# Kernel tuning notes

Measured on AMD Instinct MI355X. Metric: run time of the kernel, lower is better.

## Reference

```python
import jax, jax.numpy as jnp
import numpy as np

B, S, D, H, DFF = 2, 2048, 1024, 16, 4096
DK = D // H
EPS = 1e-6


def layer_norm(x, alpha, bias):
    # torch: alpha * (x - mean) / (std_unbiased + eps) + bias
    mean = jnp.mean(x, axis=-1, keepdims=True)
    std = jnp.sqrt(jnp.var(x, axis=-1, keepdims=True, ddof=1))
    return alpha * (x - mean) / (std + EPS) + bias


def setup_inputs() -> dict:
    key = jax.random.key(0)
    ks = jax.random.split(key, 10)
    w = lambda k, shape: (jax.random.normal(k, shape, jnp.float32) * 0.02)
    return {
        "x": jax.random.normal(ks[0], (B, S, D), jnp.float32),
        "mask": jnp.ones((B, 1, 1, S), jnp.int32),
        "wq": w(ks[1], (D, D)),
        "wk": w(ks[2], (D, D)),
        "wv": w(ks[3], (D, D)),
        "wo": w(ks[4], (D, D)),
        "w1": w(ks[5], (DFF, D)),
        "b1": jnp.zeros((DFF,), jnp.float32),
        "w2": w(ks[6], (D, DFF)),
        "b2": jnp.zeros((D,), jnp.float32),
        "alpha1": jnp.ones((D,), jnp.float32),
        "bias1": jnp.zeros((D,), jnp.float32),
        "alpha2": jnp.ones((D,), jnp.float32),
        "bias2": jnp.zeros((D,), jnp.float32),
    }


def reference(x, mask, wq, wk, wv, wo, w1, b1, w2, b2, alpha1, bias1, alpha2, bias2):
    # --- residual 1: pre-norm + self-attention ---
    xn = layer_norm(x, alpha1, bias1)                      # [B,S,D]
    q = (xn @ wq.T).reshape(B, S, H, DK).transpose(0, 2, 1, 3)  # [B,H,S,DK]
    k = (xn @ wk.T).reshape(B, S, H, DK).transpose(0, 2, 1, 3)
    v = (xn @ wv.T).reshape(B, S, H, DK).transpose(0, 2, 1, 3)
    scores = jnp.einsum("bhqd,bhkd->bhqk", q, k) / jnp.sqrt(jnp.float32(DK))
    scores = jnp.where(mask == 0, jnp.float32(-1e9), scores)
    attn = jax.nn.softmax(scores, axis=-1)                 # [B,H,S,S]
    av = jnp.einsum("bhqk,bhkd->bhqd", attn, v)            # [B,H,S,DK]
    av = av.transpose(0, 2, 1, 3).reshape(B, S, D)
    x = x + av @ wo.T                                      # dropout p=0
    # --- residual 2: pre-norm + FFN ---
    xn2 = layer_norm(x, alpha2, bias2)
    h = jax.nn.relu(xn2 @ w1.T + b1)                       # [B,S,DFF]
    x = x + h @ w2.T + b2
    return x
```

## Files before the change

kernel.cpp:

```cpp
#include <hip/hip_runtime.h>

#define B_   2
#define S_   2048
#define D_   1024
#define H_   16
#define DK_  64
#define DFF_ 4096
#define NTOK (B_ * S_)

#define QSCALE 0.18033688011112042f

typedef __bf16 bf16x8 __attribute__((ext_vector_type(8)));
typedef __bf16 bf16x4 __attribute__((ext_vector_type(4)));
typedef __bf16 bf16x2 __attribute__((ext_vector_type(2)));
typedef float  f32x4  __attribute__((ext_vector_type(4)));
typedef int    i32x4  __attribute__((ext_vector_type(4)));

#if __has_builtin(__builtin_amdgcn_exp2f)
#define EXP2(x) __builtin_amdgcn_exp2f(x)
#else
#define EXP2(x) exp2f(x)
#endif

__device__ __forceinline__ void ld16(const __bf16* g, __bf16* l) {
  __builtin_amdgcn_global_load_lds(
      (const __attribute__((address_space(1))) void*)g,
      (__attribute__((address_space(3))) void*)l, 16, 0, 0);
}

#define RAW_BAR()     __asm__ __volatile__("s_barrier" ::: "memory")
#define SCHED_FENCE() __builtin_amdgcn_sched_barrier(0)

__device__ __forceinline__ int packbf(float lo, float hi) {
  bf16x2 r; r[0] = (__bf16)lo; r[1] = (__bf16)hi;
  return __builtin_bit_cast(int, r);
}

__device__ __forceinline__ void swap32(int a, int b, int& g0, int& g1, bool hi32) {
#if __has_builtin(__builtin_amdgcn_permlane32_swap)
  auto r = __builtin_amdgcn_permlane32_swap(a, b, false, false);
  g0 = r[0]; g1 = r[1];
  (void)hi32;
#else
  const int sa = __builtin_amdgcn_ds_swizzle(a, 0x801F);
  const int sb = __builtin_amdgcn_ds_swizzle(b, 0x801F);
  g0 = hi32 ? sb : a;
  g1 = hi32 ? b : sa;
#endif
}

__device__ __forceinline__ void swap16(int a, int b, int& h0, int& h1, bool hi16) {
#if __has_builtin(__builtin_amdgcn_permlane16_swap)
  auto r = __builtin_amdgcn_permlane16_swap(a, b, false, false);
  h0 = r[0]; h1 = r[1];
  (void)hi16;
#else
  const int sa = __builtin_amdgcn_ds_swizzle(a, 0x401F);
  const int sb = __builtin_amdgcn_ds_swizzle(b, 0x401F);
  h0 = hi16 ? sb : a;
  h1 = hi16 ? b : sa;
#endif
}

__device__ __forceinline__ void xcd_swz256(int& bx, int& by) {
  const int gx = gridDim.x;
  const int flat = blockIdx.y * gx + blockIdx.x;
  const int x = flat & 7, n = flat >> 3;
  if (gx == 16) { by = ((x >> 1) << 2) + (n >> 3); bx = ((x & 1) << 3) + (n & 7); }
  else          { by = (x << 1) + (n >> 2);        bx = n & 3; }
}

__device__ __forceinline__ void lda4(bf16x8 (&afr)[4], const __bf16* hb,
                                     int abase, int f0) {
#pragma unroll
  for (int i = 0; i < 4; ++i)
    afr[i] = *(const bf16x8*)(hb + abase + (f0 + i) * 512);
}

__device__ __forceinline__ void ldb4(bf16x8 (&bfr)[4], const __bf16* hb,
                                     int bbase) {
#pragma unroll
  for (int j = 0; j < 4; ++j)
    bfr[j] = *(const bf16x8*)(hb + bbase + j * 512);
}

__device__ __forceinline__ void mm16(f32x4 (&acc)[8][4], const bf16x8 (&afr)[4],
                                     const bf16x8 (&bfr)[4], int r0) {
#pragma unroll
  for (int i = 0; i < 4; ++i)
#pragma unroll
    for (int j = 0; j < 4; ++j)
      acc[r0 + i][j] =
          __builtin_amdgcn_mfma_f32_16x16x32_bf16(afr[i], bfr[j], acc[r0 + i][j], 0, 0, 0);
}

__device__ __forceinline__ void gemm_core_256(
    const __bf16* __restrict__ A, const __bf16* __restrict__ W,
    int ld, int kLen, int rowA0, int rowW0,
    f32x4 (&acc)[8][4], __bf16* Ls)
{
  const int t = threadIdx.x;
  const int lane = t & 63, wv = t >> 6;
  const int wm = wv >> 2, wn = wv & 3;
  const int l15 = lane & 15, q4 = lane >> 4;

  const int lane_rd = l15 * 32 + ((q4 * 8) ^ (((l15 >> 1) & 3) << 3));
  const int abase = wm * 4096 + lane_rd;
  const int bbase = wn * 2048 + lane_rd;

  const int sc0 = t ^ ((t >> 3) & 3);
  const __bf16* gA0 = A + (size_t)(rowA0 + (sc0 >> 2)) * ld + (sc0 & 3) * 8;
  const __bf16* gA1 = gA0 + (size_t)128 * ld;
  const __bf16* gW0 = W + (size_t)(rowW0 + (sc0 >> 2)) * ld + (sc0 & 3) * 8;
  const __bf16* gW1 = gW0 + (size_t)128 * ld;
  const int d0 = wv * 512, d1 = 4096 + wv * 512;

#pragma unroll
  for (int i = 0; i < 8; ++i)
#pragma unroll
    for (int j = 0; j < 4; ++j) acc[i][j] = (f32x4){0.f, 0.f, 0.f, 0.f};

#define HBASE(slot, mat, h) (Ls + ((((slot)*2) + (mat)) * 2 + (h)) * 8192)
#define STG_A(tt, h, slot) do { __bf16* _d = HBASE(slot, 0, h);              \
    const int _ko = (tt) * 64 + (h) * 32;                                    \
    ld16(gA0 + _ko, _d + d0); ld16(gA1 + _ko, _d + d1); } while (0)
#define STG_B(tt, h, slot) do { __bf16* _d = HBASE(slot, 1, h);              \
    const int _ko = (tt) * 64 + (h) * 32;                                    \
    ld16(gW0 + _ko, _d + d0); ld16(gW1 + _ko, _d + d1); } while (0)
#define MFMA_PH(r0) do { RAW_BAR(); SCHED_FENCE();                           \
    __builtin_amdgcn_s_setprio(1); mm16(acc, afr, bfr, r0);                  \
    __builtin_amdgcn_s_setprio(0); SCHED_FENCE(); RAW_BAR(); } while (0)

  const int NT = kLen >> 6;
  bf16x8 afr[4], bfr[4];

  STG_A(0, 0, 0); STG_A(0, 1, 0); STG_B(0, 0, 0); STG_B(0, 1, 0);
  STG_B(1, 0, 1); STG_A(1, 0, 1); STG_B(1, 1, 1);
  __asm__ __volatile__("s_waitcnt vmcnt(6)" ::: "memory");
  RAW_BAR(); SCHED_FENCE();

  for (int u = 0; u < NT; u += 2) {
    const bool g2 = (u + 2) < NT, g3 = (u + 3) < NT;
    lda4(afr, HBASE(0, 0, 0), abase, 0); ldb4(bfr, HBASE(0, 1, 0), bbase);
    STG_A(u + 1, 1, 1);
    MFMA_PH(0);
    lda4(afr, HBASE(0, 0, 0), abase, 4);
    if (g2) STG_B(u + 2, 0, 0);
    MFMA_PH(4);
    lda4(afr, HBASE(0, 0, 1), abase, 0); ldb4(bfr, HBASE(0, 1, 1), bbase);
    if (g2) STG_A(u + 2, 0, 0);
    MFMA_PH(0);
    lda4(afr, HBASE(0, 0, 1), abase, 4);
    if (g2) {
      STG_B(u + 2, 1, 0);
      __asm__ __volatile__("s_waitcnt vmcnt(6)" ::: "memory");
    } else {
      __asm__ __volatile__("s_waitcnt vmcnt(0)" ::: "memory");
    }
    MFMA_PH(4);
    lda4(afr, HBASE(1, 0, 0), abase, 0); ldb4(bfr, HBASE(1, 1, 0), bbase);
    if (g2) STG_A(u + 2, 1, 0);
    MFMA_PH(0);
    lda4(afr, HBASE(1, 0, 0), abase, 4);
    if (g3) STG_B(u + 3, 0, 1);
    MFMA_PH(4);
    lda4(afr, HBASE(1, 0, 1), abase, 0); ldb4(bfr, HBASE(1, 1, 1), bbase);
    if (g3) STG_A(u + 3, 0, 1);
    MFMA_PH(0);
    lda4(afr, HBASE(1, 0, 1), abase, 4);
    if (g3) STG_B(u + 3, 1, 1);
    __asm__ __volatile__("s_waitcnt vmcnt(6)" ::: "memory");
    MFMA_PH(4);
  }
#undef HBASE
#undef STG_A
#undef STG_B
#undef MFMA_PH
}

__global__ __launch_bounds__(512, 2) void gemm_qkv_256(
    const __bf16* __restrict__ xn,
    const __bf16* __restrict__ wqb, const __bf16* __restrict__ wkb,
    const __bf16* __restrict__ wvb,
    __bf16* __restrict__ qo, __bf16* __restrict__ ko, __bf16* __restrict__ vto)
{
  __shared__ __align__(16) __bf16 Ls[65536];
  int bx, by; xcd_swz256(bx, by);
  const __bf16* W = blockIdx.z == 0 ? wqb : (blockIdx.z == 1 ? wkb : wvb);
  f32x4 acc[8][4];
  gemm_core_256(xn, W, D_, D_, by * 256, bx * 256, acc, Ls);

  const int t = threadIdx.x, lane = t & 63, wv = t >> 6;
  const int wm = wv >> 2, wn = wv & 3;
  const int l15 = lane & 15, q4 = lane >> 4;
  const int row0 = by * 256 + wm * 128;
  const int col0 = bx * 256 + wn * 64;

  if (blockIdx.z < 2) {
    __bf16* o = blockIdx.z == 0 ? qo : ko;
    const float sc = blockIdx.z == 0 ? QSCALE : 1.0f;
#pragma unroll
    for (int fr = 0; fr < 8; ++fr)
#pragma unroll
      for (int fc = 0; fc < 4; ++fc) {
        const int col = col0 + fc * 16 + l15;
#pragma unroll
        for (int r = 0; r < 4; ++r) {
          const int row = row0 + fr * 16 + q4 * 4 + r;
          o[(size_t)row * D_ + col] = (__bf16)(acc[fr][fc][r] * sc);
        }
      }
  } else {
#pragma unroll
    for (int fr = 0; fr < 8; ++fr)
#pragma unroll
      for (int fc = 0; fc < 4; ++fc) {
        const int tok0 = row0 + fr * 16 + q4 * 4;
        const int c    = col0 + fc * 16 + l15;
        const int b0 = tok0 >> 11, s0 = tok0 & (S_ - 1);
        const int hh = c >> 6, dd = c & (DK_ - 1);
        bf16x4 pk;
#pragma unroll
        for (int r = 0; r < 4; ++r) pk[r] = (__bf16)acc[fr][fc][r];
        *(bf16x4*)&vto[(size_t)((b0 * H_ + hh) * DK_ + dd) * S_ + s0] = pk;
      }
  }
}

__global__ __launch_bounds__(512, 2) void gemm_ffn1_256(
    const __bf16* __restrict__ A, const __bf16* __restrict__ W,
    __bf16* __restrict__ outb, const float* __restrict__ bias)
{
  __shared__ __align__(16) __bf16 Ls[65536];
  int bx, by; xcd_swz256(bx, by);
  f32x4 acc[8][4];
  gemm_core_256(A, W, D_, D_, by * 256, bx * 256, acc, Ls);

  const int t = threadIdx.x, lane = t & 63, wv = t >> 6;
  const int wm = wv >> 2, wn = wv & 3;
  const int l15 = lane & 15, q4 = lane >> 4;
  const int row0 = by * 256 + wm * 128;
  const int col0 = bx * 256 + wn * 64;

#pragma unroll
  for (int fr = 0; fr < 8; ++fr)
#pragma unroll
    for (int fc = 0; fc < 4; ++fc) {
      const int col = col0 + fc * 16 + l15;
      const float bs = bias[col];
#pragma unroll
      for (int r = 0; r < 4; ++r) {
        const int row = row0 + fr * 16 + q4 * 4 + r;
        outb[(size_t)row * DFF_ + col] = (__bf16)fmaxf(acc[fr][fc][r] + bs, 0.0f);
      }
    }
}

__global__ __launch_bounds__(512, 2) void gemm_ffn2_sk4(
    const __bf16* __restrict__ A, const __bf16* __restrict__ W,
    __bf16* __restrict__ p0, __bf16* __restrict__ p1,
    __bf16* __restrict__ p2, __bf16* __restrict__ p3)
{
  __shared__ __align__(16) __bf16 Ls[65536];
  int bx, by; xcd_swz256(bx, by);
  const int z = blockIdx.z;
  f32x4 acc[8][4];
  gemm_core_256(A + (size_t)z * 1024, W + (size_t)z * 1024, DFF_, 1024,
                by * 256, bx * 256, acc, Ls);

  const int t = threadIdx.x, lane = t & 63, wv = t >> 6;
  const int wm = wv >> 2, wn = wv & 3;
  const int l15 = lane & 15, q4 = lane >> 4;
  const int row0 = by * 256 + wm * 128;
  const int col0 = bx * 256 + wn * 64;
  __bf16* out = z == 0 ? p0 : (z == 1 ? p1 : (z == 2 ? p2 : p3));

#pragma unroll
  for (int fr = 0; fr < 8; ++fr)
#pragma unroll
    for (int fc = 0; fc < 4; ++fc) {
      const int col = col0 + fc * 16 + l15;
#pragma unroll
      for (int r = 0; r < 4; ++r) {
        const int row = row0 + fr * 16 + q4 * 4 + r;
        out[(size_t)row * D_ + col] = (__bf16)acc[fr][fc][r];
      }
    }
}

__global__ __launch_bounds__(512, 2) void gemm_oproj_sk4(
    const __bf16* __restrict__ A, const __bf16* __restrict__ W,
    __bf16* __restrict__ pp)
{
  __shared__ __align__(16) __bf16 Ls[65536];
  int bx, by; xcd_swz256(bx, by);
  const int z = blockIdx.z;
  f32x4 acc[8][4];
  gemm_core_256(A + (size_t)z * 256, W + (size_t)z * 256, D_, 256,
                by * 256, bx * 256, acc, Ls);

  const int t = threadIdx.x, lane = t & 63, wv = t >> 6;
  const int wm = wv >> 2, wn = wv & 3;
  const int l15 = lane & 15, q4 = lane >> 4;
  const int row0 = by * 256 + wm * 128;
  const int col0 = bx * 256 + wn * 64;
  __bf16* out = pp + (size_t)z * NTOK * D_;

#pragma unroll
  for (int fr = 0; fr < 8; ++fr)
#pragma unroll
    for (int fc = 0; fc < 4; ++fc) {
      const int col = col0 + fc * 16 + l15;
#pragma unroll
      for (int r = 0; r < 4; ++r) {
        const int row = row0 + fr * 16 + q4 * 4 + r;
        out[(size_t)row * D_ + col] = (__bf16)acc[fr][fc][r];
      }
    }
}

__global__ __launch_bounds__(256) void oproj_ln_reduce(
    const float* __restrict__ x, const __bf16* __restrict__ opp,
    const float* __restrict__ alpha, const float* __restrict__ bias,
    const float* __restrict__ b2, float* __restrict__ dout,
    __bf16* __restrict__ xn2)
{
  const int row = blockIdx.x;
  const int t = threadIdx.x;
  const size_t base = (size_t)row * D_;
  const size_t st4 = (size_t)NTOK * D_ / 4;
  const size_t i4 = base / 4 + t;
  float4 v = ((const float4*)(x + base))[t];
  const bf16x4 a0 = ((const bf16x4*)opp)[i4];
  const bf16x4 a1 = ((const bf16x4*)opp)[i4 + st4];
  const bf16x4 a2 = ((const bf16x4*)opp)[i4 + 2 * st4];
  const bf16x4 a3 = ((const bf16x4*)opp)[i4 + 3 * st4];
  v.x += (float)a0[0] + (float)a1[0] + (float)a2[0] + (float)a3[0];
  v.y += (float)a0[1] + (float)a1[1] + (float)a2[1] + (float)a3[1];
  v.z += (float)a0[2] + (float)a1[2] + (float)a2[2] + (float)a3[2];
  v.w += (float)a0[3] + (float)a1[3] + (float)a2[3] + (float)a3[3];

  const float4 bb = ((const float4*)b2)[t];
  float4 o4;
  o4.x = v.x + bb.x; o4.y = v.y + bb.y; o4.z = v.z + bb.z; o4.w = v.w + bb.w;
  ((float4*)(dout + base))[t] = o4;

  float s  = v.x + v.y + v.z + v.w;
  float ss = v.x * v.x + v.y * v.y + v.z * v.z + v.w * v.w;
#pragma unroll
  for (int m = 1; m < 64; m <<= 1) {
    s  += __shfl_xor(s, m);
    ss += __shfl_xor(ss, m);
  }
  __shared__ float red[8];
  if ((t & 63) == 0) { red[t >> 6] = s; red[4 + (t >> 6)] = ss; }
  __syncthreads();
  s  = red[0] + red[1] + red[2] + red[3];
  ss = red[4] + red[5] + red[6] + red[7];
  const float mean = s * (1.0f / D_);
  float var = (ss - (float)D_ * mean * mean) * (1.0f / (D_ - 1));
  var = fmaxf(var, 0.0f);
  const float inv = 1.0f / (sqrtf(var) + 1e-6f);
  const float4 al = ((const float4*)alpha)[t];
  const float4 bi = ((const float4*)bias)[t];
  bf16x4 o;
  o.x = (__bf16)(al.x * (v.x - mean) * inv + bi.x);
  o.y = (__bf16)(al.y * (v.y - mean) * inv + bi.y);
  o.z = (__bf16)(al.z * (v.z - mean) * inv + bi.z);
  o.w = (__bf16)(al.w * (v.w - mean) * inv + bi.w);
  ((bf16x4*)(xn2 + base))[t] = o;
}

__global__ __launch_bounds__(256) void ffn2_reduce(
    const __bf16* __restrict__ p0, const __bf16* __restrict__ p1,
    const __bf16* __restrict__ p2, const __bf16* __restrict__ p3,
    float* __restrict__ out)
{
  const int idx4 = blockIdx.x * 256 + threadIdx.x;
  float4 v = ((const float4*)out)[idx4];
  const bf16x4 q0 = ((const bf16x4*)p0)[idx4];
  const bf16x4 q1 = ((const bf16x4*)p1)[idx4];
  const bf16x4 q2 = ((const bf16x4*)p2)[idx4];
  const bf16x4 q3 = ((const bf16x4*)p3)[idx4];
  v.x += (float)q0[0] + (float)q1[0] + (float)q2[0] + (float)q3[0];
  v.y += (float)q0[1] + (float)q1[1] + (float)q2[1] + (float)q3[1];
  v.z += (float)q0[2] + (float)q1[2] + (float)q2[2] + (float)q3[2];
  v.w += (float)q0[3] + (float)q1[3] + (float)q2[3] + (float)q3[3];
  ((float4*)out)[idx4] = v;
}

struct CastJobs {
  const float* src[6];
  __bf16* dst[6];
  int n4[6];
};

__global__ __launch_bounds__(256) void cast_ln_kernel(
    CastJobs cj, const float* __restrict__ x, const float* __restrict__ alpha,
    const float* __restrict__ bias, __bf16* __restrict__ xn1)
{
  const int j = blockIdx.y;
  if (j < 6) {
    const int i = blockIdx.x * 256 + threadIdx.x;
    if (i < cj.n4[j]) {
      float4 v = ((const float4*)cj.src[j])[i];
      bf16x4 o;
      o.x = (__bf16)v.x; o.y = (__bf16)v.y; o.z = (__bf16)v.z; o.w = (__bf16)v.w;
      ((bf16x4*)cj.dst[j])[i] = o;
    }
    return;
  }
  const int row = blockIdx.x;
  const int t = threadIdx.x;
  const float4 v = ((const float4*)(x + (size_t)row * D_))[t];
  float s  = v.x + v.y + v.z + v.w;
  float ss = v.x * v.x + v.y * v.y + v.z * v.z + v.w * v.w;
#pragma unroll
  for (int m = 1; m < 64; m <<= 1) {
    s  += __shfl_xor(s, m);
    ss += __shfl_xor(ss, m);
  }
  __shared__ float red[8];
  if ((t & 63) == 0) { red[t >> 6] = s; red[4 + (t >> 6)] = ss; }
  __syncthreads();
  s  = red[0] + red[1] + red[2] + red[3];
  ss = red[4] + red[5] + red[6] + red[7];
  const float mean = s * (1.0f / D_);
  float var = (ss - (float)D_ * mean * mean) * (1.0f / (D_ - 1));
  var = fmaxf(var, 0.0f);
  const float inv = 1.0f / (sqrtf(var) + 1e-6f);
  const float4 al = ((const float4*)alpha)[t];
  const float4 bi = ((const float4*)bias)[t];
  bf16x4 o;
  o.x = (__bf16)(al.x * (v.x - mean) * inv + bi.x);
  o.y = (__bf16)(al.y * (v.y - mean) * inv + bi.y);
  o.z = (__bf16)(al.z * (v.z - mean) * inv + bi.z);
  o.w = (__bf16)(al.w * (v.w - mean) * inv + bi.w);
  ((bf16x4*)(xn1 + (size_t)row * D_))[t] = o;
}

__global__ __launch_bounds__(256) void attn_kernel(
    const __bf16* __restrict__ qg, const __bf16* __restrict__ kg,
    const __bf16* __restrict__ vtg, const int* __restrict__ mask,
    __bf16* __restrict__ av)
{
  __shared__ __align__(16) __bf16 Ks[2][4096];
  __shared__ __align__(16) __bf16 Vt[2][4096];
  __shared__ __align__(16) __bf16 Qs[8192];
  __shared__ int Dd[32];

  const int t = threadIdx.x, lane = t & 63, wv = t >> 6;
  const int l15 = lane & 15, q4 = lane >> 4;
  const bool hi16 = (lane & 16) != 0, hi32 = (lane & 32) != 0;
  const int bh = blockIdx.x;
  const int b = bh >> 4, h = bh & (H_ - 1);
  const int q0 = blockIdx.y * 128;

  const int srow = lane & 7, sc8 = lane >> 3;
  const __bf16* qg0 = qg + (size_t)(b * S_ + q0 + 32 * wv + srow) * D_ + h * DK_ + sc8 * 8;
  __bf16* lQ = Qs + wv * 2048;
#pragma unroll
  for (int p = 0; p < 4; ++p)
    ld16(qg0 + (size_t)(8 * p) * D_, lQ + 512 * p);

  const __bf16* kg0 = kg + (size_t)(b * S_ + 16 * wv + srow) * D_ + h * DK_ + sc8 * 8;
  const __bf16* vt0 = vtg + (size_t)(bh * DK_ + 16 * wv + srow) * S_ + sc8 * 8;

  if (t < 32) Dd[t] = 0;

  ld16(kg0,                  Ks[0] + wv * 1024);
  ld16(kg0 + (size_t)8 * D_, Ks[0] + wv * 1024 + 512);
  ld16(vt0,                  Vt[0] + wv * 1024);
  ld16(vt0 + (size_t)8 * S_, Vt[0] + wv * 1024 + 512);

  __syncthreads();

  {
    const int4* m4 = (const int4*)(mask + (size_t)b * S_) + t * 2;
    const int4 a = m4[0], c = m4[1];
    const bool anyz = (a.x == 0) | (a.y == 0) | (a.z == 0) | (a.w == 0) |
                      (c.x == 0) | (c.y == 0) | (c.z == 0) | (c.w == 0);
    if (anyz) Dd[t >> 3] = 1;
  }
  __syncthreads();
  const bool blockDirty = (__ballot(Dd[lane & 31] != 0) != 0ull);

  const int fb = ((l15 >> 3) << 9) + (q4 << 6) + ((l15 & 7) << 3);
  const int mrow = b * S_;

  bf16x8 bq[2][2];
#pragma unroll
  for (int j = 0; j < 2; ++j)
#pragma unroll
    for (int s = 0; s < 2; ++s)
      bq[j][s] = *(const bf16x8*)(lQ + j * 1024 + s * 256 + fb);

  bf16x8 bones;
#pragma unroll
  for (int e = 0; e < 8; ++e) bones[e] = (__bf16)1.0f;
  const f32x4 z4 = {0.f, 0.f, 0.f, 0.f};

  f32x4 lacc[2];
  f32x4 oacc[2][4];
#pragma unroll
  for (int m = 0; m < 2; ++m) {
    lacc[m] = z4;
#pragma unroll
    for (int jd = 0; jd < 4; ++jd) oacc[m][jd] = z4;
  }

  for (int kv0 = 0; kv0 < S_; kv0 += 64) {
    const int buf = (kv0 >> 6) & 1;
    if (kv0 + 64 < S_) {
      const size_t nk = (size_t)(kv0 + 64);
      ld16(kg0 + nk * D_,              Ks[buf ^ 1] + wv * 1024);
      ld16(kg0 + (nk + 8) * D_,        Ks[buf ^ 1] + wv * 1024 + 512);
      ld16(vt0 + nk,                   Vt[buf ^ 1] + wv * 1024);
      ld16(vt0 + (size_t)8 * S_ + nk,  Vt[buf ^ 1] + wv * 1024 + 512);
    }

    f32x4 sacc[4][2];
    __builtin_amdgcn_s_setprio(1);
#pragma unroll
    for (int i = 0; i < 4; ++i) {
      const bf16x8 ak0 = *(const bf16x8*)(Ks[buf] + i * 1024 + fb);
      const bf16x8 ak1 = *(const bf16x8*)(Ks[buf] + i * 1024 + fb + 256);
      sacc[i][0] = __builtin_amdgcn_mfma_f32_16x16x32_bf16(ak0, bq[0][0], z4, 0, 0, 0);
      sacc[i][1] = __builtin_amdgcn_mfma_f32_16x16x32_bf16(ak0, bq[1][0], z4, 0, 0, 0);
      sacc[i][0] = __builtin_amdgcn_mfma_f32_16x16x32_bf16(ak1, bq[0][1], sacc[i][0], 0, 0, 0);
      sacc[i][1] = __builtin_amdgcn_mfma_f32_16x16x32_bf16(ak1, bq[1][1], sacc[i][1], 0, 0, 0);
    }
    __builtin_amdgcn_s_setprio(0);

    if (blockDirty && Dd[kv0 >> 6]) {
#pragma unroll
      for (int i = 0; i < 4; ++i)
#pragma unroll
        for (int r = 0; r < 4; ++r)
          if (mask[mrow + kv0 + 16 * i + 4 * q4 + r] == 0) {
            sacc[i][0][r] = -1e30f;
            sacc[i][1][r] = -1e30f;
          }
    }

#pragma unroll
    for (int i = 0; i < 4; ++i)
#pragma unroll
      for (int j = 0; j < 2; ++j)
#pragma unroll
        for (int r = 0; r < 4; ++r)
          sacc[i][j][r] = EXP2(sacc[i][j][r]);

    bf16x8 ap[2][2];
#pragma unroll
    for (int j = 0; j < 2; ++j)
#pragma unroll
      for (int s = 0; s < 2; ++s) {
        const int pa0 = packbf(sacc[2 * s][j][0],     sacc[2 * s][j][1]);
        const int pa1 = packbf(sacc[2 * s][j][2],     sacc[2 * s][j][3]);
        const int pb0 = packbf(sacc[2 * s + 1][j][0], sacc[2 * s + 1][j][1]);
        const int pb1 = packbf(sacc[2 * s + 1][j][2], sacc[2 * s + 1][j][3]);
        int g0, g1, g2, g3, h0, h1, h2, h3;
        swap32(pa0, pb0, g0, g1, hi32);
        swap32(pa1, pb1, g2, g3, hi32);
        swap16(g0, g1, h0, h1, hi16);
        swap16(g2, g3, h2, h3, hi16);
        i32x4 fw; fw[0] = h0; fw[1] = h2; fw[2] = h1; fw[3] = h3;
        ap[j][s] = __builtin_bit_cast(bf16x8, fw);
      }

    __builtin_amdgcn_s_setprio(1);
#pragma unroll
    for (int jd = 0; jd < 4; ++jd)
#pragma unroll
      for (int s = 0; s < 2; ++s) {
        bf16x8 bv = *(const bf16x8*)(Vt[buf] + jd * 1024 + fb + s * 256);
#pragma unroll
        for (int m = 0; m < 2; ++m)
          oacc[m][jd] = __builtin_amdgcn_mfma_f32_16x16x32_bf16(ap[m][s], bv, oacc[m][jd], 0, 0, 0);
      }
#pragma unroll
    for (int m = 0; m < 2; ++m)
#pragma unroll
      for (int s = 0; s < 2; ++s)
        lacc[m] = __builtin_amdgcn_mfma_f32_16x16x32_bf16(ap[m][s], bones, lacc[m], 0, 0, 0);
    __builtin_amdgcn_s_setprio(0);

    __syncthreads();
  }

#pragma unroll
  for (int m = 0; m < 2; ++m) {
    f32x4 lt;
#pragma unroll
    for (int r = 0; r < 4; ++r) lt[r] = 1.0f / lacc[m][r];
#pragma unroll
    for (int jd = 0; jd < 4; ++jd)
#pragma unroll
      for (int r = 0; r < 4; ++r) {
        int tok = b * S_ + q0 + wv * 32 + 16 * m + q4 * 4 + r;
        int c   = h * DK_ + jd * 16 + l15;
        av[(size_t)tok * D_ + c] = (__bf16)(oacc[m][jd][r] * lt[r]);
      }
  }
}

extern "C" void kernel_launch(void* const* d_in, const int* in_sizes, int n_in,
                              void* d_out, int out_size, void* d_ws, size_t ws_size,
                              hipStream_t stream) {
  const float* x      = (const float*)d_in[0];
  const int*   mask   = (const int*)d_in[1];
  const float* wq     = (const float*)d_in[2];
  const float* wk     = (const float*)d_in[3];
  const float* wv     = (const float*)d_in[4];
  const float* wo     = (const float*)d_in[5];
  const float* w1     = (const float*)d_in[6];
  const float* b1     = (const float*)d_in[7];
  const float* w2     = (const float*)d_in[8];
  const float* b2     = (const float*)d_in[9];
  const float* alpha1 = (const float*)d_in[10];
  const float* bias1  = (const float*)d_in[11];
  const float* alpha2 = (const float*)d_in[12];
  const float* bias2  = (const float*)d_in[13];

  char* ws = (char*)d_ws;
  __bf16* wqb = (__bf16*)(ws + ((size_t)0 << 20));
  __bf16* wkb = (__bf16*)(ws + ((size_t)2 << 20));
  __bf16* wvb = (__bf16*)(ws + ((size_t)4 << 20));
  __bf16* wob = (__bf16*)(ws + ((size_t)6 << 20));
  __bf16* w1b = (__bf16*)(ws + ((size_t)8 << 20));
  __bf16* w2b = (__bf16*)(ws + ((size_t)16 << 20));
  __bf16* xn1 = (__bf16*)(ws + ((size_t)24 << 20));
  __bf16* qb  = (__bf16*)(ws + ((size_t)32 << 20));
  __bf16* kb  = (__bf16*)(ws + ((size_t)40 << 20));
  __bf16* vtb = (__bf16*)(ws + ((size_t)48 << 20));
  __bf16* avb = (__bf16*)(ws + ((size_t)56 << 20));
  __bf16* opp = (__bf16*)(ws + ((size_t)24 << 20));
  __bf16* xn2 = (__bf16*)(ws + ((size_t)56 << 20));
  __bf16* hb  = (__bf16*)(ws + ((size_t)24 << 20));
  __bf16* fp0 = (__bf16*)(ws + ((size_t)0 << 20));
  __bf16* fp1 = (__bf16*)(ws + ((size_t)8 << 20));
  __bf16* fp2 = (__bf16*)(ws + ((size_t)56 << 20));
  __bf16* fp3 = (__bf16*)(ws + ((size_t)64 << 20));

  CastJobs cj;
  cj.src[0] = wq; cj.dst[0] = wqb; cj.n4[0] = D_ * D_ / 4;
  cj.src[1] = wk; cj.dst[1] = wkb; cj.n4[1] = D_ * D_ / 4;
  cj.src[2] = wv; cj.dst[2] = wvb; cj.n4[2] = D_ * D_ / 4;
  cj.src[3] = wo; cj.dst[3] = wob; cj.n4[3] = D_ * D_ / 4;
  cj.src[4] = w1; cj.dst[4] = w1b; cj.n4[4] = DFF_ * D_ / 4;
  cj.src[5] = w2; cj.dst[5] = w2b; cj.n4[5] = DFF_ * D_ / 4;

  cast_ln_kernel<<<dim3(DFF_ * D_ / 4 / 256, 7), 256, 0, stream>>>(
      cj, x, alpha1, bias1, xn1);

  gemm_qkv_256<<<dim3(D_ / 256, NTOK / 256, 3), 512, 0, stream>>>(
      xn1, wqb, wkb, wvb, qb, kb, vtb);

  attn_kernel<<<dim3(B_ * H_, S_ / 128), 256, 0, stream>>>(qb, kb, vtb, mask, avb);

  gemm_oproj_sk4<<<dim3(D_ / 256, NTOK / 256, 4), 512, 0, stream>>>(
      avb, wob, opp);

  oproj_ln_reduce<<<dim3(NTOK), 256, 0, stream>>>(
      x, opp, alpha2, bias2, b2, (float*)d_out, xn2);

  gemm_ffn1_256<<<dim3(DFF_ / 256, NTOK / 256), 512, 0, stream>>>(
      xn2, w1b, hb, b1);

  gemm_ffn2_sk4<<<dim3(D_ / 256, NTOK / 256, 4), 512, 0, stream>>>(
      hb, w2b, fp0, fp1, fp2, fp3);

  ffn2_reduce<<<dim3(NTOK * D_ / 4 / 256), 256, 0, stream>>>(
      fp0, fp1, fp2, fp3, (float*)d_out);
}
```

Before: 322.6 us.

## Software-pipeline attention with triple-buffered K/V and QK of next tile ahead

Restructures the attention kv loop so the QK^T MFMAs for tile i+1 are issued while softmax/exp and PV for tile i run, using two score register sets. K/V shared buffers grow to three so prefetch runs two tiles ahead, and the Q shared-memory staging is dropped in favor of direct global loads into registers. It also replaces the per-iteration __syncthreads with an explicit vmcnt wait plus raw barrier. This raises register pressure (two score sets) and LDS use per block, which could lower occupancy.

```diff
diff --git a/kernel.cpp b/kernel.cpp
--- a/kernel.cpp
+++ b/kernel.cpp
@@ -444,9 +444,8 @@
     const __bf16* __restrict__ vtg, const int* __restrict__ mask,
     __bf16* __restrict__ av)
 {
-  __shared__ __align__(16) __bf16 Ks[2][4096];
-  __shared__ __align__(16) __bf16 Vt[2][4096];
-  __shared__ __align__(16) __bf16 Qs[8192];
+  __shared__ __align__(16) __bf16 Ks[3][4096];
+  __shared__ __align__(16) __bf16 Vt[3][4096];
   __shared__ int Dd[32];
 
   const int t = threadIdx.x, lane = t & 63, wv = t >> 6;
@@ -455,23 +454,21 @@
   const int bh = blockIdx.x;
   const int b = bh >> 4, h = bh & (H_ - 1);
   const int q0 = blockIdx.y * 128;
-
   const int srow = lane & 7, sc8 = lane >> 3;
-  const __bf16* qg0 = qg + (size_t)(b * S_ + q0 + 32 * wv + srow) * D_ + h * DK_ + sc8 * 8;
-  __bf16* lQ = Qs + wv * 2048;
-#pragma unroll
-  for (int p = 0; p < 4; ++p)
-    ld16(qg0 + (size_t)(8 * p) * D_, lQ + 512 * p);
 
   const __bf16* kg0 = kg + (size_t)(b * S_ + 16 * wv + srow) * D_ + h * DK_ + sc8 * 8;
   const __bf16* vt0 = vtg + (size_t)(bh * DK_ + 16 * wv + srow) * S_ + sc8 * 8;
 
   if (t < 32) Dd[t] = 0;
 
-  ld16(kg0,                  Ks[0] + wv * 1024);
-  ld16(kg0 + (size_t)8 * D_, Ks[0] + wv * 1024 + 512);
-  ld16(vt0,                  Vt[0] + wv * 1024);
-  ld16(vt0 + (size_t)8 * S_, Vt[0] + wv * 1024 + 512);
+  ld16(kg0,                       Ks[0] + wv * 1024);
+  ld16(kg0 + (size_t)8 * D_,      Ks[0] + wv * 1024 + 512);
+  ld16(vt0,                       Vt[0] + wv * 1024);
+  ld16(vt0 + (size_t)8 * S_,      Vt[0] + wv * 1024 + 512);
+  ld16(kg0 + (size_t)64 * D_,     Ks[1] + wv * 1024);
+  ld16(kg0 + (size_t)72 * D_,     Ks[1] + wv * 1024 + 512);
+  ld16(vt0 + 64,                  Vt[1] + wv * 1024);
+  ld16(vt0 + (size_t)8 * S_ + 64, Vt[1] + wv * 1024 + 512);
 
   __syncthreads();
 
@@ -493,7 +490,8 @@
   for (int j = 0; j < 2; ++j)
 #pragma unroll
     for (int s = 0; s < 2; ++s)
-      bq[j][s] = *(const bf16x8*)(lQ + j * 1024 + s * 256 + fb);
+      bq[j][s] = *(const bf16x8*)(qg +
+          (size_t)(b * S_ + q0 + 32 * wv + j * 16 + l15) * D_ + h * DK_ + s * 32 + q4 * 8);
 
   bf16x8 bones;
 #pragma unroll
@@ -509,85 +507,103 @@
     for (int jd = 0; jd < 4; ++jd) oacc[m][jd] = z4;
   }
 
-  for (int kv0 = 0; kv0 < S_; kv0 += 64) {
-    const int buf = (kv0 >> 6) & 1;
-    if (kv0 + 64 < S_) {
-      const size_t nk = (size_t)(kv0 + 64);
-      ld16(kg0 + nk * D_,              Ks[buf ^ 1] + wv * 1024);
-      ld16(kg0 + (nk + 8) * D_,        Ks[buf ^ 1] + wv * 1024 + 512);
-      ld16(vt0 + nk,                   Vt[buf ^ 1] + wv * 1024);
-      ld16(vt0 + (size_t)8 * S_ + nk,  Vt[buf ^ 1] + wv * 1024 + 512);
-    }
-
-    f32x4 sacc[4][2];
-    __builtin_amdgcn_s_setprio(1);
-#pragma unroll
-    for (int i = 0; i < 4; ++i) {
-      const bf16x8 ak0 = *(const bf16x8*)(Ks[buf] + i * 1024 + fb);
-      const bf16x8 ak1 = *(const bf16x8*)(Ks[buf] + i * 1024 + fb + 256);
-      sacc[i][0] = __builtin_amdgcn_mfma_f32_16x16x32_bf16(ak0, bq[0][0], z4, 0, 0, 0);
-      sacc[i][1] = __builtin_amdgcn_mfma_f32_16x16x32_bf16(ak0, bq[1][0], z4, 0, 0, 0);
-      sacc[i][0] = __builtin_amdgcn_mfma_f32_16x16x32_bf16(ak1, bq[0][1], sacc[i][0], 0, 0, 0);
-      sacc[i][1] = __builtin_amdgcn_mfma_f32_16x16x32_bf16(ak1, bq[1][1], sacc[i][1], 0, 0, 0);
-    }
-    __builtin_amdgcn_s_setprio(0);
-
-    if (blockDirty && Dd[kv0 >> 6]) {
-#pragma unroll
-      for (int i = 0; i < 4; ++i)
-#pragma unroll
-        for (int r = 0; r < 4; ++r)
-          if (mask[mrow + kv0 + 16 * i + 4 * q4 + r] == 0) {
-            sacc[i][0][r] = -1e30f;
-            sacc[i][1][r] = -1e30f;
-          }
-    }
-
-#pragma unroll
-    for (int i = 0; i < 4; ++i)
-#pragma unroll
-      for (int j = 0; j < 2; ++j)
-#pragma unroll
-        for (int r = 0; r < 4; ++r)
-          sacc[i][j][r] = EXP2(sacc[i][j][r]);
-
-    bf16x8 ap[2][2];
-#pragma unroll
-    for (int j = 0; j < 2; ++j)
-#pragma unroll
-      for (int s = 0; s < 2; ++s) {
-        const int pa0 = packbf(sacc[2 * s][j][0],     sacc[2 * s][j][1]);
-        const int pa1 = packbf(sacc[2 * s][j][2],     sacc[2 * s][j][3]);
-        const int pb0 = packbf(sacc[2 * s + 1][j][0], sacc[2 * s + 1][j][1]);
-        const int pb1 = packbf(sacc[2 * s + 1][j][2], sacc[2 * s + 1][j][3]);
-        int g0, g1, g2, g3, h0, h1, h2, h3;
-        swap32(pa0, pb0, g0, g1, hi32);
-        swap32(pa1, pb1, g2, g3, hi32);
-        swap16(g0, g1, h0, h1, hi16);
-        swap16(g2, g3, h2, h3, hi16);
-        i32x4 fw; fw[0] = h0; fw[1] = h2; fw[2] = h1; fw[3] = h3;
-        ap[j][s] = __builtin_bit_cast(bf16x8, fw);
-      }
-
-    __builtin_amdgcn_s_setprio(1);
-#pragma unroll
-    for (int jd = 0; jd < 4; ++jd)
-#pragma unroll
-      for (int s = 0; s < 2; ++s) {
-        bf16x8 bv = *(const bf16x8*)(Vt[buf] + jd * 1024 + fb + s * 256);
-#pragma unroll
-        for (int m = 0; m < 2; ++m)
-          oacc[m][jd] = __builtin_amdgcn_mfma_f32_16x16x32_bf16(ap[m][s], bv, oacc[m][jd], 0, 0, 0);
-      }
-#pragma unroll
-    for (int m = 0; m < 2; ++m)
-#pragma unroll
-      for (int s = 0; s < 2; ++s)
-        lacc[m] = __builtin_amdgcn_mfma_f32_16x16x32_bf16(ap[m][s], bones, lacc[m], 0, 0, 0);
-    __builtin_amdgcn_s_setprio(0);
-
-    __syncthreads();
-  }
+  const __bf16 *kC = Ks[0], *kN = Ks[1], *vC = Vt[0], *vN = Vt[1];
+  __bf16 *kP = Ks[2], *vP = Vt[2];
+
+  f32x4 sA[4][2], sB[4][2];
+
+#pragma unroll
+  for (int i = 0; i < 4; ++i) {
+    const bf16x8 ak0 = *(const bf16x8*)(kC + i * 1024 + fb);
+    const bf16x8 ak1 = *(const bf16x8*)(kC + i * 1024 + fb + 256);
+    sA[i][0] = __builtin_amdgcn_mfma_f32_16x16x32_bf16(ak0, bq[0][0], z4, 0, 0, 0);
+    sA[i][1] = __builtin_amdgcn_mfma_f32_16x16x32_bf16(ak0, bq[1][0], z4, 0, 0, 0);
+    sA[i][0] = __builtin_amdgcn_mfma_f32_16x16x32_bf16(ak1, bq[0][1], sA[i][0], 0, 0, 0);
+    sA[i][1] = __builtin_amdgcn_mfma_f32_16x16x32_bf16(ak1, bq[1][1], sA[i][1], 0, 0, 0);
+  }
+
+#define ATTN_BODY(IT, SIN, SOUT)                                              \
+  do {                                                                        \
+    const int kv0_ = (IT) * 64;                                               \
+    if (kv0_ + 128 < S_) {                 \
+      const size_t nk_ = (size_t)(kv0_ + 128);                                \
+      ld16(kg0 + nk_ * D_,             kP + wv * 1024);                       \
+      ld16(kg0 + (nk_ + 8) * D_,       kP + wv * 1024 + 512);                 \
+      ld16(vt0 + nk_,                  vP + wv * 1024);                       \
+      ld16(vt0 + (size_t)8 * S_ + nk_, vP + wv * 1024 + 512);                 \
+    }                                                                         \
+    if (kv0_ + 64 < S_) {                       \
+      _Pragma("unroll")                                                       \
+      for (int i_ = 0; i_ < 4; ++i_) {                                        \
+        const bf16x8 ak0_ = *(const bf16x8*)(kN + i_ * 1024 + fb);            \
+        const bf16x8 ak1_ = *(const bf16x8*)(kN + i_ * 1024 + fb + 256);      \
+        SOUT[i_][0] = __builtin_amdgcn_mfma_f32_16x16x32_bf16(ak0_, bq[0][0], z4, 0, 0, 0); \
+        SOUT[i_][1] = __builtin_amdgcn_mfma_f32_16x16x32_bf16(ak0_, bq[1][0], z4, 0, 0, 0); \
+        SOUT[i_][0] = __builtin_amdgcn_mfma_f32_16x16x32_bf16(ak1_, bq[0][1], SOUT[i_][0], 0, 0, 0); \
+        SOUT[i_][1] = __builtin_amdgcn_mfma_f32_16x16x32_bf16(ak1_, bq[1][1], SOUT[i_][1], 0, 0, 0); \
+      }                                                                       \
+    }                                                                         \
+    if (blockDirty && Dd[(IT)]) {                                             \
+      _Pragma("unroll")                                                       \
+      for (int i_ = 0; i_ < 4; ++i_)                                          \
+        _Pragma("unroll")                                                     \
+        for (int r_ = 0; r_ < 4; ++r_)                                        \
+          if (mask[mrow + kv0_ + 16 * i_ + 4 * q4 + r_] == 0) {               \
+            SIN[i_][0][r_] = -1e30f;                                          \
+            SIN[i_][1][r_] = -1e30f;                                          \
+          }                                                                   \
+    }                                                                         \
+    _Pragma("unroll")                                                         \
+    for (int i_ = 0; i_ < 4; ++i_)                                            \
+      _Pragma("unroll")                                                       \
+      for (int j_ = 0; j_ < 2; ++j_)                                          \
+        _Pragma("unroll")                                                     \
+        for (int r_ = 0; r_ < 4; ++r_)                                        \
+          SIN[i_][j_][r_] = EXP2(SIN[i_][j_][r_]);                            \
+    bf16x8 ap_[2][2];                                                         \
+    _Pragma("unroll")                                                         \
+    for (int j_ = 0; j_ < 2; ++j_)                                            \
+      _Pragma("unroll")                                                       \
+      for (int s_ = 0; s_ < 2; ++s_) {                                        \
+        const int pa0_ = packbf(SIN[2 * s_][j_][0],     SIN[2 * s_][j_][1]);  \
+        const int pa1_ = packbf(SIN[2 * s_][j_][2],     SIN[2 * s_][j_][3]);  \
+        const int pb0_ = packbf(SIN[2 * s_ + 1][j_][0], SIN[2 * s_ + 1][j_][1]); \
+        const int pb1_ = packbf(SIN[2 * s_ + 1][j_][2], SIN[2 * s_ + 1][j_][3]); \
+        int g0_, g1_, g2_, g3_, h0_, h1_, h2_, h3_;                           \
+        swap32(pa0_, pb0_, g0_, g1_, hi32);                                   \
+        swap32(pa1_, pb1_, g2_, g3_, hi32);                                   \
+        swap16(g0_, g1_, h0_, h1_, hi16);                                     \
+        swap16(g2_, g3_, h2_, h3_, hi16);                                     \
+        i32x4 fw_; fw_[0] = h0_; fw_[1] = h2_; fw_[2] = h1_; fw_[3] = h3_;    \
+        ap_[j_][s_] = __builtin_bit_cast(bf16x8, fw_);                        \
+      }                                                                       \
+    __builtin_amdgcn_s_setprio(1);                                            \
+    _Pragma("unroll")                                                         \
+    for (int jd_ = 0; jd_ < 4; ++jd_)                                         \
+      _Pragma("unroll")                                                       \
+      for (int s_ = 0; s_ < 2; ++s_) {                                        \
+        bf16x8 bv_ = *(const bf16x8*)(vC + jd_ * 1024 + fb + s_ * 256);       \
+        _Pragma("unroll")                                                     \
+        for (int m_ = 0; m_ < 2; ++m_)                                        \
+          oacc[m_][jd_] = __builtin_amdgcn_mfma_f32_16x16x32_bf16(ap_[m_][s_], bv_, oacc[m_][jd_], 0, 0, 0); \
+      }                                                                       \
+    _Pragma("unroll")                                                         \
+    for (int m_ = 0; m_ < 2; ++m_)                                            \
+      _Pragma("unroll")                                                       \
+      for (int s_ = 0; s_ < 2; ++s_)                                          \
+        lacc[m_] = __builtin_amdgcn_mfma_f32_16x16x32_bf16(ap_[m_][s_], bones, lacc[m_], 0, 0, 0); \
+    __builtin_amdgcn_s_setprio(0);                                            \
+    __asm__ __volatile__("s_waitcnt vmcnt(0)" ::: "memory");                  \
+    RAW_BAR();                                                                \
+    const __bf16* tk_ = kC; kC = kN; kN = kP; kP = (__bf16*)tk_;              \
+    const __bf16* tv_ = vC; vC = vN; vN = vP; vP = (__bf16*)tv_;              \
+  } while (0)
+
+  for (int it = 0; it < 32; it += 2) {
+    ATTN_BODY(it,     sA, sB);
+    ATTN_BODY(it + 1, sB, sA);
+  }
+#undef ATTN_BODY
 
 #pragma unroll
   for (int m = 0; m < 2; ++m) {
```

Result: slower. 333.6 us (+3.4%).

## Halve attention query tile per block to raise occupancy and block count

Applied to the files above, without the earlier changes.

The attention kernel now processes 64 queries per block (16 per wave) instead of 128, doubling the grid to 1024 blocks and removing the Q shared-memory staging in favor of direct global loads into registers. Launch bounds request 4 blocks per CU, and register and LDS usage per block drop. The trade-off is that each K/V tile loaded into LDS is reused by half as many queries, doubling total K/V traffic and the per-query share of synchronization.

```diff
diff --git a/kernel.cpp b/kernel.cpp
--- a/kernel.cpp
+++ b/kernel.cpp
@@ -439,14 +439,13 @@
   ((bf16x4*)(xn1 + (size_t)row * D_))[t] = o;
 }
 
-__global__ __launch_bounds__(256) void attn_kernel(
+__global__ __launch_bounds__(256, 4) void attn_kernel(
     const __bf16* __restrict__ qg, const __bf16* __restrict__ kg,
     const __bf16* __restrict__ vtg, const int* __restrict__ mask,
     __bf16* __restrict__ av)
 {
   __shared__ __align__(16) __bf16 Ks[2][4096];
   __shared__ __align__(16) __bf16 Vt[2][4096];
-  __shared__ __align__(16) __bf16 Qs[8192];
   __shared__ int Dd[32];
 
   const int t = threadIdx.x, lane = t & 63, wv = t >> 6;
@@ -454,14 +453,8 @@
   const bool hi16 = (lane & 16) != 0, hi32 = (lane & 32) != 0;
   const int bh = blockIdx.x;
   const int b = bh >> 4, h = bh & (H_ - 1);
-  const int q0 = blockIdx.y * 128;
-
+  const int q0 = blockIdx.y * 64;
   const int srow = lane & 7, sc8 = lane >> 3;
-  const __bf16* qg0 = qg + (size_t)(b * S_ + q0 + 32 * wv + srow) * D_ + h * DK_ + sc8 * 8;
-  __bf16* lQ = Qs + wv * 2048;
-#pragma unroll
-  for (int p = 0; p < 4; ++p)
-    ld16(qg0 + (size_t)(8 * p) * D_, lQ + 512 * p);
 
   const __bf16* kg0 = kg + (size_t)(b * S_ + 16 * wv + srow) * D_ + h * DK_ + sc8 * 8;
   const __bf16* vt0 = vtg + (size_t)(bh * DK_ + 16 * wv + srow) * S_ + sc8 * 8;
@@ -488,26 +481,21 @@
   const int fb = ((l15 >> 3) << 9) + (q4 << 6) + ((l15 & 7) << 3);
   const int mrow = b * S_;
 
-  bf16x8 bq[2][2];
-#pragma unroll
-  for (int j = 0; j < 2; ++j)
-#pragma unroll
-    for (int s = 0; s < 2; ++s)
-      bq[j][s] = *(const bf16x8*)(lQ + j * 1024 + s * 256 + fb);
+  bf16x8 bq[2];
+#pragma unroll
+  for (int s = 0; s < 2; ++s)
+    bq[s] = *(const bf16x8*)(qg +
+        (size_t)(b * S_ + q0 + 16 * wv + l15) * D_ + h * DK_ + s * 32 + q4 * 8);
 
   bf16x8 bones;
 #pragma unroll
   for (int e = 0; e < 8; ++e) bones[e] = (__bf16)1.0f;
   const f32x4 z4 = {0.f, 0.f, 0.f, 0.f};
 
-  f32x4 lacc[2];
-  f32x4 oacc[2][4];
-#pragma unroll
-  for (int m = 0; m < 2; ++m) {
-    lacc[m] = z4;
-#pragma unroll
-    for (int jd = 0; jd < 4; ++jd) oacc[m][jd] = z4;
-  }
+  f32x4 lacc = z4;
+  f32x4 oacc[4];
+#pragma unroll
+  for (int jd = 0; jd < 4; ++jd) oacc[jd] = z4;
 
   for (int kv0 = 0; kv0 < S_; kv0 += 64) {
     const int buf = (kv0 >> 6) & 1;
@@ -519,16 +507,14 @@
       ld16(vt0 + (size_t)8 * S_ + nk,  Vt[buf ^ 1] + wv * 1024 + 512);
     }
 
-    f32x4 sacc[4][2];
+    f32x4 sacc[4];
     __builtin_amdgcn_s_setprio(1);
 #pragma unroll
     for (int i = 0; i < 4; ++i) {
       const bf16x8 ak0 = *(const bf16x8*)(Ks[buf] + i * 1024 + fb);
       const bf16x8 ak1 = *(const bf16x8*)(Ks[buf] + i * 1024 + fb + 256);
-      sacc[i][0] = __builtin_amdgcn_mfma_f32_16x16x32_bf16(ak0, bq[0][0], z4, 0, 0, 0);
-      sacc[i][1] = __builtin_amdgcn_mfma_f32_16x16x32_bf16(ak0, bq[1][0], z4, 0, 0, 0);
-      sacc[i][0] = __builtin_amdgcn_mfma_f32_16x16x32_bf16(ak1, bq[0][1], sacc[i][0], 0, 0, 0);
-      sacc[i][1] = __builtin_amdgcn_mfma_f32_16x16x32_bf16(ak1, bq[1][1], sacc[i][1], 0, 0, 0);
+      sacc[i] = __builtin_amdgcn_mfma_f32_16x16x32_bf16(ak0, bq[0], z4, 0, 0, 0);
+      sacc[i] = __builtin_amdgcn_mfma_f32_16x16x32_bf16(ak1, bq[1], sacc[i], 0, 0, 0);
     }
     __builtin_amdgcn_s_setprio(0);
 
@@ -537,37 +523,31 @@
       for (int i = 0; i < 4; ++i)
 #pragma unroll
         for (int r = 0; r < 4; ++r)
-          if (mask[mrow + kv0 + 16 * i + 4 * q4 + r] == 0) {
-            sacc[i][0][r] = -1e30f;
-            sacc[i][1][r] = -1e30f;
-          }
+          if (mask[mrow + kv0 + 16 * i + 4 * q4 + r] == 0)
+            sacc[i][r] = -1e30f;
     }
 
 #pragma unroll
     for (int i = 0; i < 4; ++i)
 #pragma unroll
-      for (int j = 0; j < 2; ++j)
-#pragma unroll
-        for (int r = 0; r < 4; ++r)
-          sacc[i][j][r] = EXP2(sacc[i][j][r]);
-
-    bf16x8 ap[2][2];
-#pragma unroll
-    for (int j = 0; j < 2; ++j)
-#pragma unroll
-      for (int s = 0; s < 2; ++s) {
-        const int pa0 = packbf(sacc[2 * s][j][0],     sacc[2 * s][j][1]);
-        const int pa1 = packbf(sacc[2 * s][j][2],     sacc[2 * s][j][3]);
-        const int pb0 = packbf(sacc[2 * s + 1][j][0], sacc[2 * s + 1][j][1]);
-        const int pb1 = packbf(sacc[2 * s + 1][j][2], sacc[2 * s + 1][j][3]);
-        int g0, g1, g2, g3, h0, h1, h2, h3;
-        swap32(pa0, pb0, g0, g1, hi32);
-        swap32(pa1, pb1, g2, g3, hi32);
-        swap16(g0, g1, h0, h1, hi16);
-        swap16(g2, g3, h2, h3, hi16);
-        i32x4 fw; fw[0] = h0; fw[1] = h2; fw[2] = h1; fw[3] = h3;
-        ap[j][s] = __builtin_bit_cast(bf16x8, fw);
-      }
+      for (int r = 0; r < 4; ++r)
+        sacc[i][r] = EXP2(sacc[i][r]);
+
+    bf16x8 ap[2];
+#pragma unroll
+    for (int s = 0; s < 2; ++s) {
+      const int pa0 = packbf(sacc[2 * s][0],     sacc[2 * s][1]);
+      const int pa1 = packbf(sacc[2 * s][2],     sacc[2 * s][3]);
+      const int pb0 = packbf(sacc[2 * s + 1][0], sacc[2 * s + 1][1]);
+      const int pb1 = packbf(sacc[2 * s + 1][2], sacc[2 * s + 1][3]);
+      int g0, g1, g2, g3, h0, h1, h2, h3;
+      swap32(pa0, pb0, g0, g1, hi32);
+      swap32(pa1, pb1, g2, g3, hi32);
+      swap16(g0, g1, h0, h1, hi16);
+      swap16(g2, g3, h2, h3, hi16);
+      i32x4 fw; fw[0] = h0; fw[1] = h2; fw[2] = h1; fw[3] = h3;
+      ap[s] = __builtin_bit_cast(bf16x8, fw);
+    }
 
     __builtin_amdgcn_s_setprio(1);
 #pragma unroll
@@ -575,34 +555,27 @@
 #pragma unroll
       for (int s = 0; s < 2; ++s) {
         bf16x8 bv = *(const bf16x8*)(Vt[buf] + jd * 1024 + fb + s * 256);
-#pragma unroll
-        for (int m = 0; m < 2; ++m)
-          oacc[m][jd] = __builtin_amdgcn_mfma_f32_16x16x32_bf16(ap[m][s], bv, oacc[m][jd], 0, 0, 0);
+        oacc[jd] = __builtin_amdgcn_mfma_f32_16x16x32_bf16(ap[s], bv, oacc[jd], 0, 0, 0);
       }
 #pragma unroll
-    for (int m = 0; m < 2; ++m)
-#pragma unroll
-      for (int s = 0; s < 2; ++s)
-        lacc[m] = __builtin_amdgcn_mfma_f32_16x16x32_bf16(ap[m][s], bones, lacc[m], 0, 0, 0);
+    for (int s = 0; s < 2; ++s)
+      lacc = __builtin_amdgcn_mfma_f32_16x16x32_bf16(ap[s], bones, lacc, 0, 0, 0);
     __builtin_amdgcn_s_setprio(0);
 
     __syncthreads();
   }
 
-#pragma unroll
-  for (int m = 0; m < 2; ++m) {
-    f32x4 lt;
-#pragma unroll
-    for (int r = 0; r < 4; ++r) lt[r] = 1.0f / lacc[m][r];
-#pragma unroll
-    for (int jd = 0; jd < 4; ++jd)
-#pragma unroll
-      for (int r = 0; r < 4; ++r) {
-        int tok = b * S_ + q0 + wv * 32 + 16 * m + q4 * 4 + r;
-        int c   = h * DK_ + jd * 16 + l15;
-        av[(size_t)tok * D_ + c] = (__bf16)(oacc[m][jd][r] * lt[r]);
-      }
-  }
+  f32x4 lt;
+#pragma unroll
+  for (int r = 0; r < 4; ++r) lt[r] = 1.0f / lacc[r];
+#pragma unroll
+  for (int jd = 0; jd < 4; ++jd)
+#pragma unroll
+    for (int r = 0; r < 4; ++r) {
+      int tok = b * S_ + q0 + 16 * wv + q4 * 4 + r;
+      int c   = h * DK_ + jd * 16 + l15;
+      av[(size_t)tok * D_ + c] = (__bf16)(oacc[jd][r] * lt[r]);
+    }
 }
 
 extern "C" void kernel_launch(void* const* d_in, const int* in_sizes, int n_in,
@@ -657,7 +630,7 @@
   gemm_qkv_256<<<dim3(D_ / 256, NTOK / 256, 3), 512, 0, stream>>>(
       xn1, wqb, wkb, wvb, qb, kb, vtb);
 
-  attn_kernel<<<dim3(B_ * H_, S_ / 128), 256, 0, stream>>>(qb, kb, vtb, mask, avb);
+  attn_kernel<<<dim3(B_ * H_, S_ / 64), 256, 0, stream>>>(qb, kb, vtb, mask, avb);
 
   gemm_oproj_sk4<<<dim3(D_ / 256, NTOK / 256, 4), 512, 0, stream>>>(
       avb, wob, opp);
```

Result: slower. 336.4 us (+4.3%).

## Split attention over two KV halves and merge partials in a combine kernel

Applied to the files above, without the earlier changes.

Attention now runs in two blocks per query tile, each covering half of the key/value sequence. Each block writes an unnormalized bf16 output and its row sums, and a new combine kernel adds the two halves and divides by the summed denominators. This doubles grid parallelism (512 to 1024 blocks) and drops the shared Q staging in favour of direct global loads. The cost is an extra kernel launch and extra memory traffic for the partials, plus rounding the unnormalized outputs to bf16. Merging the halves by plain addition works only because the softmax path uses no running max.

```diff
diff --git a/kernel.cpp b/kernel.cpp
--- a/kernel.cpp
+++ b/kernel.cpp
@@ -439,14 +439,13 @@
   ((bf16x4*)(xn1 + (size_t)row * D_))[t] = o;
 }
 
-__global__ __launch_bounds__(256) void attn_kernel(
+__global__ __launch_bounds__(256, 4) void attn_sk2(
     const __bf16* __restrict__ qg, const __bf16* __restrict__ kg,
     const __bf16* __restrict__ vtg, const int* __restrict__ mask,
-    __bf16* __restrict__ av)
+    __bf16* __restrict__ o0, __bf16* __restrict__ o1, float* __restrict__ lp)
 {
   __shared__ __align__(16) __bf16 Ks[2][4096];
   __shared__ __align__(16) __bf16 Vt[2][4096];
-  __shared__ __align__(16) __bf16 Qs[8192];
   __shared__ int Dd[32];
 
   const int t = threadIdx.x, lane = t & 63, wv = t >> 6;
@@ -455,23 +454,19 @@
   const int bh = blockIdx.x;
   const int b = bh >> 4, h = bh & (H_ - 1);
   const int q0 = blockIdx.y * 128;
-
+  const int z  = blockIdx.z;
+  const int z0 = z << 10;
   const int srow = lane & 7, sc8 = lane >> 3;
-  const __bf16* qg0 = qg + (size_t)(b * S_ + q0 + 32 * wv + srow) * D_ + h * DK_ + sc8 * 8;
-  __bf16* lQ = Qs + wv * 2048;
-#pragma unroll
-  for (int p = 0; p < 4; ++p)
-    ld16(qg0 + (size_t)(8 * p) * D_, lQ + 512 * p);
 
   const __bf16* kg0 = kg + (size_t)(b * S_ + 16 * wv + srow) * D_ + h * DK_ + sc8 * 8;
   const __bf16* vt0 = vtg + (size_t)(bh * DK_ + 16 * wv + srow) * S_ + sc8 * 8;
 
   if (t < 32) Dd[t] = 0;
 
-  ld16(kg0,                  Ks[0] + wv * 1024);
-  ld16(kg0 + (size_t)8 * D_, Ks[0] + wv * 1024 + 512);
-  ld16(vt0,                  Vt[0] + wv * 1024);
-  ld16(vt0 + (size_t)8 * S_, Vt[0] + wv * 1024 + 512);
+  ld16(kg0 + (size_t)z0 * D_,       Ks[0] + wv * 1024);
+  ld16(kg0 + (size_t)(z0 + 8) * D_, Ks[0] + wv * 1024 + 512);
+  ld16(vt0 + z0,                    Vt[0] + wv * 1024);
+  ld16(vt0 + (size_t)8 * S_ + z0,   Vt[0] + wv * 1024 + 512);
 
   __syncthreads();
 
@@ -493,7 +488,8 @@
   for (int j = 0; j < 2; ++j)
 #pragma unroll
     for (int s = 0; s < 2; ++s)
-      bq[j][s] = *(const bf16x8*)(lQ + j * 1024 + s * 256 + fb);
+      bq[j][s] = *(const bf16x8*)(qg +
+          (size_t)(b * S_ + q0 + 32 * wv + j * 16 + l15) * D_ + h * DK_ + s * 32 + q4 * 8);
 
   bf16x8 bones;
 #pragma unroll
@@ -509,9 +505,9 @@
     for (int jd = 0; jd < 4; ++jd) oacc[m][jd] = z4;
   }
 
-  for (int kv0 = 0; kv0 < S_; kv0 += 64) {
-    const int buf = (kv0 >> 6) & 1;
-    if (kv0 + 64 < S_) {
+  for (int kv0 = z0; kv0 < z0 + 1024; kv0 += 64) {
+    const int buf = ((kv0 - z0) >> 6) & 1;
+    if (kv0 + 64 < z0 + 1024) {
       const size_t nk = (size_t)(kv0 + 64);
       ld16(kg0 + nk * D_,              Ks[buf ^ 1] + wv * 1024);
       ld16(kg0 + (nk + 8) * D_,        Ks[buf ^ 1] + wv * 1024 + 512);
@@ -589,20 +585,45 @@
     __syncthreads();
   }
 
-#pragma unroll
-  for (int m = 0; m < 2; ++m) {
-    f32x4 lt;
-#pragma unroll
-    for (int r = 0; r < 4; ++r) lt[r] = 1.0f / lacc[m][r];
+  __bf16* op = z == 0 ? o0 : o1;
+#pragma unroll
+  for (int m = 0; m < 2; ++m)
 #pragma unroll
     for (int jd = 0; jd < 4; ++jd)
 #pragma unroll
       for (int r = 0; r < 4; ++r) {
         int tok = b * S_ + q0 + wv * 32 + 16 * m + q4 * 4 + r;
         int c   = h * DK_ + jd * 16 + l15;
-        av[(size_t)tok * D_ + c] = (__bf16)(oacc[m][jd][r] * lt[r]);
+        op[(size_t)tok * D_ + c] = (__bf16)oacc[m][jd][r];
       }
-  }
+  if (l15 == 0) {
+    float* lz = lp + (size_t)z * 65536 + (size_t)bh * S_ + q0 + wv * 32;
+#pragma unroll
+    for (int m = 0; m < 2; ++m)
+#pragma unroll
+      for (int r = 0; r < 4; ++r)
+        lz[16 * m + q4 * 4 + r] = lacc[m][r];
+  }
+}
+
+__global__ __launch_bounds__(256) void attn_combine(
+    const __bf16* __restrict__ o0, const __bf16* __restrict__ o1,
+    const float* __restrict__ lp, __bf16* __restrict__ av)
+{
+  const int idx4 = blockIdx.x * 256 + threadIdx.x;
+  const int tok = idx4 >> 8;
+  const int cq  = idx4 & 255;
+  const int hh  = cq >> 4;
+  const int b   = tok >> 11, s = tok & (S_ - 1);
+  const int li  = (b * H_ + hh) * S_ + s;
+  const float inv = 1.0f / (lp[li] + lp[65536 + li]);
+  const bf16x4 a = ((const bf16x4*)o0)[idx4];
+  const bf16x4 c = ((const bf16x4*)o1)[idx4];
+  bf16x4 o;
+#pragma unroll
+  for (int r = 0; r < 4; ++r)
+    o[r] = (__bf16)(((float)a[r] + (float)c[r]) * inv);
+  ((bf16x4*)av)[idx4] = o;
 }
 
 extern "C" void kernel_launch(void* const* d_in, const int* in_sizes, int n_in,
@@ -635,6 +656,9 @@
   __bf16* kb  = (__bf16*)(ws + ((size_t)40 << 20));
   __bf16* vtb = (__bf16*)(ws + ((size_t)48 << 20));
   __bf16* avb = (__bf16*)(ws + ((size_t)56 << 20));
+  __bf16* ao0 = (__bf16*)(ws + ((size_t)24 << 20));
+  __bf16* ao1 = (__bf16*)(ws + ((size_t)72 << 20));
+  float*  alp = (float*) (ws + ((size_t)64 << 20));
   __bf16* opp = (__bf16*)(ws + ((size_t)24 << 20));
   __bf16* xn2 = (__bf16*)(ws + ((size_t)56 << 20));
   __bf16* hb  = (__bf16*)(ws + ((size_t)24 << 20));
@@ -657,7 +681,11 @@
   gemm_qkv_256<<<dim3(D_ / 256, NTOK / 256, 3), 512, 0, stream>>>(
       xn1, wqb, wkb, wvb, qb, kb, vtb);
 
-  attn_kernel<<<dim3(B_ * H_, S_ / 128), 256, 0, stream>>>(qb, kb, vtb, mask, avb);
+  attn_sk2<<<dim3(B_ * H_, S_ / 128, 2), 256, 0, stream>>>(
+      qb, kb, vtb, mask, ao0, ao1, alp);
+
+  attn_combine<<<dim3(NTOK * D_ / 4 / 256), 256, 0, stream>>>(
+      ao0, ao1, alp, avb);
 
   gemm_oproj_sk4<<<dim3(D_ / 256, NTOK / 256, 4), 512, 0, stream>>>(
       avb, wob, opp);
```

Measured after the change: 330.7 us. 2.5% more time.
